# Kernel tuning notes

Hardware: AMD Instinct MI355X
Metric: run time of the kernel (lower is better)

The kernel has to match this reference:

```python
import jax, jax.numpy as jnp
import numpy as np

NUM_OBJECTS = 6          # self.NUM_OBJECTS
SCORE_THRESH = 1e-4      # self.score_tresh
NMS_THRESHS = jnp.asarray(np.arange(0.001, 1.0, 0.1), dtype=jnp.float32)  # 10 thresholds
K_CAND = 1024            # fixed-shape cap on (proposal,class) candidates per image
CLASS_OFFSET = 4096.0    # > max image coord; batched_nms per-class offset trick


def _iou_matrix(b):
    # b: [K,4] xyxy -> [K,K] IoU
    x1, y1, x2, y2 = b[:, 0], b[:, 1], b[:, 2], b[:, 3]
    area = (x2 - x1) * (y2 - y1)
    iw = jnp.clip(jnp.minimum(x2[:, None], x2[None, :]) - jnp.maximum(x1[:, None], x1[None, :]), 0.0)
    ih = jnp.clip(jnp.minimum(y2[:, None], y2[None, :]) - jnp.maximum(y1[:, None], y1[None, :]), 0.0)
    inter = iw * ih
    union = area[:, None] + area[None, :] - inter
    return jnp.where(union > 0, inter / union, 0.0)


def _greedy_nms(iou, valid, thresh):
    # candidates are pre-sorted by descending score; sequential greedy suppression
    K = valid.shape[0]
    ar = jnp.arange(K)
    def body(i, keep):
        sup = keep[i] & (iou[i] > thresh) & (ar > i)
        return keep & ~sup
    return jax.lax.fori_loop(0, K, body, valid)


def _per_image(logits, boxes, feats, hw):
    # logits [N,81], boxes [N,80,4], feats [N,2048], hw [2] (h,w)
    C = boxes.shape[1]
    probs = jax.nn.softmax(logits, axis=-1)[:, :C]          # drop background class
    h = hw[0].astype(boxes.dtype)
    w = hw[1].astype(boxes.dtype)
    b = jnp.stack([jnp.clip(boxes[..., 0], 0.0, w),         # clip to image
                   jnp.clip(boxes[..., 1], 0.0, h),
                   jnp.clip(boxes[..., 2], 0.0, w),
                   jnp.clip(boxes[..., 3], 0.0, h)], axis=-1)
    scores = probs.reshape(-1)                              # [N*C]
    vals, idx = jax.lax.top_k(jnp.where(scores > SCORE_THRESH, scores, -1.0), K_CAND)
    cand_valid = vals > SCORE_THRESH
    cb = b.reshape(-1, 4)[idx]                              # [K,4]
    cls = (idx % C).astype(boxes.dtype)
    prop = idx // C                                         # proposal row index
    iou = _iou_matrix(cb + cls[:, None] * CLASS_OFFSET)     # per-class NMS via offsets
    keeps = jax.vmap(lambda t: _greedy_nms(iou, cand_valid, t))(NMS_THRESHS)  # [T,K]
    counts = keeps.sum(axis=1)
    # torch loop: break at first (smallest) thresh yielding len(ids)==6, i.e. >=6 kept
    ok = counts >= NUM_OBJECTS
    t_sel = jnp.where(jnp.any(ok), jnp.argmax(ok), NMS_THRESHS.shape[0] - 1)
    keep = keeps[t_sel]
    _, top = jax.lax.top_k(jnp.where(keep, vals, -jnp.inf), NUM_OBJECTS)
    ids = prop[top]                                         # [6]
    return feats[ids].T                                     # [2048, 6] (permute(1,0))


def _forward(cls_logits, boxes, feature_pooled, image_hw):
    return jax.vmap(_per_image)(cls_logits, boxes, feature_pooled, image_hw)  # [B,2048,6]


def setup_inputs() -> dict:
    key = jax.random.key(0)
    k1, k2, k3, k4, k5 = jax.random.split(key, 5)
    B, N, C, D = 8, 1000, 80, 2048
    cls_logits = jax.random.normal(k1, (B, N, C + 1), dtype=jnp.float32)
    ctr = jax.random.uniform(k2, (B, N, C, 2), minval=0.0, maxval=800.0)
    sz = jax.random.uniform(k3, (B, N, C, 2), minval=8.0, maxval=200.0)
    boxes = jnp.concatenate([ctr - sz * 0.5, ctr + sz * 0.5], axis=-1).astype(jnp.float32)
    feature_pooled = jax.random.normal(k4, (B, N, D), dtype=jnp.float32)
    image_hw = jax.random.randint(k5, (B, 2), 600, 800, dtype=jnp.int32)
    return {"cls_logits": cls_logits, "boxes": boxes,
            "feature_pooled": feature_pooled, "image_hw": image_hw}


def reference(cls_logits, boxes, feature_pooled, image_hw):
    return _forward(cls_logits, boxes, feature_pooled, image_hw)
```

## Files before the change

kernel.cpp:

```cpp
#include <hip/hip_runtime.h>
#include <cmath>
#include <cstdint>

#define NB 8
#define NPROP 1000
#define NCLS 80
#define NLOG 81
#define KCAND 1024
#define NTH 10
#define DFEAT 2048
#define NOBJ 6
#define NSCORE (NPROP*NCLS)
#define HBLK 8
#define HCHUNK (NSCORE/HBLK)

constexpr size_t OFF_SCORES = 0;
constexpr size_t SZ_SCORES  = (size_t)NB * NSCORE * 4;
constexpr size_t OFF_LISTA  = OFF_SCORES + SZ_SCORES;
constexpr size_t SZ_LISTA   = (size_t)NB * 20 * KCAND * 8;
constexpr size_t OFF_H1     = OFF_LISTA;
constexpr size_t OFF_H2     = OFF_H1 + (size_t)NB * HBLK * 2048 * 4;
constexpr size_t OFF_PIV    = OFF_H2 + (size_t)NB * HBLK * 2048 * 4;
constexpr size_t OFF_CBUF   = OFF_PIV + (size_t)NB * 8 * 4;
constexpr size_t OFF_CANDK  = OFF_LISTA + SZ_LISTA;
constexpr size_t SZ_CANDK   = (size_t)NB * KCAND * 8;
constexpr size_t OFF_CX1    = OFF_CANDK + SZ_CANDK;
constexpr size_t SZ_CARR    = (size_t)NB * KCAND * 4;
constexpr size_t OFF_CY1    = OFF_CX1 + SZ_CARR;
constexpr size_t OFF_CX2    = OFF_CY1 + SZ_CARR;
constexpr size_t OFF_CY2    = OFF_CX2 + SZ_CARR;
constexpr size_t OFF_CAREA  = OFF_CY2 + SZ_CARR;
constexpr size_t OFF_CPROP  = OFF_CAREA + SZ_CARR;
constexpr size_t OFF_VALIDW = OFF_CPROP + SZ_CARR;
constexpr size_t SZ_VALIDW  = (size_t)NB * 16 * 8;
constexpr size_t OFF_MASKS  = OFF_VALIDW + SZ_VALIDW;
constexpr size_t SZ_MASKS   = (size_t)NTH * NB * KCAND * 16 * 8;
constexpr size_t OFF_KEEPS  = OFF_MASKS + SZ_MASKS;
constexpr size_t SZ_KEEPS   = (size_t)NB * NTH * 16 * 8;
constexpr size_t OFF_COUNTS = OFF_KEEPS + SZ_KEEPS;
constexpr size_t SZ_COUNTS  = (size_t)NB * NTH * 4;
constexpr size_t OFF_IDS    = OFF_COUNTS + SZ_COUNTS;

#define TSTRIDE ((size_t)NB * 16 * 1024)

__device__ __forceinline__ float nms_th(int t) {
    return (float)(0.001 + 0.1 * (double)t);
}

__device__ __forceinline__ unsigned score_vkey(float v) {
    float vv = (v > 1e-4f) ? v : -1.0f;
    unsigned bits = __float_as_uint(vv);
    unsigned u = (bits & 0x80000000u) ? ~bits : (bits | 0x80000000u);
    return ~u;
}

__global__ void k_memz(ulonglong2* __restrict__ p, int n) {
    int g = blockIdx.x * blockDim.x + threadIdx.x;
    if (g < n) p[g] = ulonglong2{0ULL, 0ULL};
}

__global__ void k_softmax(const float* __restrict__ logits, float* __restrict__ scores) {
    int wid  = (blockIdx.x * blockDim.x + threadIdx.x) >> 6;
    int lane = threadIdx.x & 63;
    if (wid >= NB * NPROP) return;
    const float* L = logits + (size_t)wid * NLOG;
    float l0 = L[lane];
    float l1 = (lane < 17) ? L[64 + lane] : -INFINITY;
    float m = fmaxf(l0, l1);
    #pragma unroll
    for (int o = 32; o > 0; o >>= 1) m = fmaxf(m, __shfl_xor(m, o, 64));
    float e0 = expf(l0 - m);
    float e1 = (lane < 17) ? expf(l1 - m) : 0.f;
    float s = e0 + e1;
    #pragma unroll
    for (int o = 32; o > 0; o >>= 1) s += __shfl_xor(s, o, 64);
    float* outp = scores + (size_t)wid * NCLS;
    outp[lane] = e0 / s;
    if (lane < 16) outp[64 + lane] = e1 / s;
}

__global__ __launch_bounds__(1024) void k_hist1(const float* __restrict__ scores,
                                                unsigned* __restrict__ hist1) {
    __shared__ unsigned hh[2048];
    int img = blockIdx.x >> 3, blk = blockIdx.x & 7;
    int tid = threadIdx.x;
    hh[tid] = 0; hh[tid + 1024] = 0;
    __syncthreads();
    const float* sc = scores + (size_t)img * NSCORE + (size_t)blk * HCHUNK;
    for (int e = tid; e < HCHUNK; e += 1024) {
        unsigned vk = score_vkey(sc[e]);
        atomicAdd(&hh[vk >> 21], 1u);
    }
    __syncthreads();
    unsigned* outp = hist1 + ((size_t)img * HBLK + blk) * 2048;
    outp[tid] = hh[tid];
    outp[tid + 1024] = hh[tid + 1024];
}

__device__ __forceinline__ void pivot_scan(const unsigned* __restrict__ h8, unsigned K,
                                           int* __restrict__ out_b, int* __restrict__ out_rem) {
    __shared__ unsigned wsum[16];
    int tid = threadIdx.x;
    unsigned a = 0, b = 0;
    #pragma unroll
    for (int s = 0; s < HBLK; ++s) {
        a += h8[s * 2048 + 2 * tid];
        b += h8[s * 2048 + 2 * tid + 1];
    }
    unsigned p = a + b;
    unsigned x = p;
    #pragma unroll
    for (int d = 1; d < 64; d <<= 1) {
        unsigned y = __shfl_up(x, (unsigned)d, 64);
        if ((tid & 63) >= d) x += y;
    }
    if ((tid & 63) == 63) wsum[tid >> 6] = x;
    __syncthreads();
    if (tid < 16) {
        unsigned w = wsum[tid];
        #pragma unroll
        for (int d = 1; d < 16; d <<= 1) {
            unsigned y = __shfl_up(w, (unsigned)d, 64);
            if (tid >= d) w += y;
        }
        wsum[tid] = w;
    }
    __syncthreads();
    unsigned wex = (tid >= 64) ? wsum[(tid >> 6) - 1] : 0u;
    unsigned incl = x + wex;
    unsigned E = incl - p;
    if (E < K && E + a >= K)              { *out_b = 2 * tid;     *out_rem = (int)(K - E); }
    else if (E + a < K && E + a + b >= K) { *out_b = 2 * tid + 1; *out_rem = (int)(K - (E + a)); }
}

__global__ __launch_bounds__(1024) void k_pivot1(const unsigned* __restrict__ hist1,
                                                 int* __restrict__ piv) {
    int img = blockIdx.x;
    pivot_scan(hist1 + (size_t)img * HBLK * 2048, KCAND,
               &piv[img * 8 + 0], &piv[img * 8 + 1]);
}

__global__ __launch_bounds__(1024) void k_hist2(const float* __restrict__ scores,
                                                const int* __restrict__ piv,
                                                unsigned* __restrict__ hist2) {
    __shared__ unsigned hh[2048];
    int img = blockIdx.x >> 3, blk = blockIdx.x & 7;
    int tid = threadIdx.x;
    hh[tid] = 0; hh[tid + 1024] = 0;
    __syncthreads();
    unsigned b1 = (unsigned)piv[img * 8 + 0];
    const float* sc = scores + (size_t)img * NSCORE + (size_t)blk * HCHUNK;
    for (int e = tid; e < HCHUNK; e += 1024) {
        unsigned vk = score_vkey(sc[e]);
        if ((vk >> 21) == b1) atomicAdd(&hh[(vk >> 10) & 2047u], 1u);
    }
    __syncthreads();
    unsigned* outp = hist2 + ((size_t)img * HBLK + blk) * 2048;
    outp[tid] = hh[tid];
    outp[tid + 1024] = hh[tid + 1024];
}

__global__ __launch_bounds__(1024) void k_pivot2(const unsigned* __restrict__ hist2,
                                                 int* __restrict__ piv) {
    __shared__ int b2s, rem2s;
    int img = blockIdx.x;
    pivot_scan(hist2 + (size_t)img * HBLK * 2048, (unsigned)piv[img * 8 + 1], &b2s, &rem2s);
    __syncthreads();
    if (threadIdx.x == 0) {
        piv[img * 8 + 2] = (piv[img * 8 + 0] << 11) | b2s;
        piv[img * 8 + 3] = 0;
    }
}

__global__ __launch_bounds__(1024) void k_gathersel(const float* __restrict__ scores,
                                                    int* __restrict__ piv,
                                                    unsigned long long* __restrict__ cbuf) {
    __shared__ unsigned lcnt, gbase;
    int img = blockIdx.x >> 3, blk = blockIdx.x & 7;
    int tid = threadIdx.x;
    if (tid == 0) lcnt = 0;
    __syncthreads();
    unsigned T22 = (unsigned)piv[img * 8 + 2];
    const float* sc = scores + (size_t)img * NSCORE + (size_t)blk * HCHUNK;
    unsigned long long sel[(HCHUNK + 1023) / 1024];
    int ns = 0;
    for (int e = tid; e < HCHUNK; e += 1024) {
        unsigned vk = score_vkey(sc[e]);
        if ((vk >> 10) <= T22)
            sel[ns++] = ((unsigned long long)vk << 32) | (unsigned)(blk * HCHUNK + e);
    }
    unsigned lp = atomicAdd(&lcnt, (unsigned)ns);
    __syncthreads();
    if (tid == 0) gbase = atomicAdd((unsigned*)&piv[img * 8 + 3], lcnt);
    __syncthreads();
    unsigned long long* ob = cbuf + (size_t)img * 2048;
    for (int i = 0; i < ns; ++i) {
        unsigned pos = gbase + lp + (unsigned)i;
        if (pos < 2048) ob[pos] = sel[i];
    }
}

__global__ __launch_bounds__(256) void k_rank(const unsigned long long* __restrict__ cbuf,
                                              const int* __restrict__ piv,
                                              unsigned long long* __restrict__ candk) {
    __shared__ unsigned long long keys[2048];
    int img = blockIdx.x >> 3, sl = blockIdx.x & 7;
    int tid = threadIdx.x;
    int cnt = piv[img * 8 + 3]; if (cnt > 2048) cnt = 2048;
    const unsigned long long* ib = cbuf + (size_t)img * 2048;
    #pragma unroll
    for (int k = 0; k < 8; ++k) {
        int t = k * 256 + tid;
        keys[t] = (t < cnt) ? ib[t] : ~0ULL;
    }
    __syncthreads();
    unsigned long long a = keys[sl * 256 + tid];
    int r = 0;
    #pragma unroll 8
    for (int j = 0; j < cnt; ++j) r += (keys[j] < a) ? 1 : 0;
    if (r < KCAND) candk[(size_t)img * KCAND + r] = a;
}

__global__ __launch_bounds__(1024) void k_cand(const unsigned long long* __restrict__ candk,
                                               const float* __restrict__ boxes,
                                               const int* __restrict__ hw,
                                               float* __restrict__ cx1, float* __restrict__ cy1,
                                               float* __restrict__ cx2, float* __restrict__ cy2,
                                               float* __restrict__ car, int* __restrict__ cprop,
                                               unsigned long long* __restrict__ validw) {
    int bimg = blockIdx.x;
    int j    = threadIdx.x;
    unsigned long long key = candk[(size_t)bimg * KCAND + j];
    unsigned int u   = ~(unsigned int)(key >> 32);
    unsigned int idx = (unsigned int)key;
    const unsigned int uth = __float_as_uint(1e-4f) | 0x80000000u;
    bool valid = u > uth;
    int prop = (int)(idx / NCLS);
    int cls  = (int)(idx - (unsigned)prop * NCLS);
    const float4 bx = *(const float4*)(boxes + ((((size_t)bimg * NPROP + prop) * NCLS + cls) << 2));
    float h = (float)hw[bimg * 2 + 0];
    float w = (float)hw[bimg * 2 + 1];
    float x1 = fminf(fmaxf(bx.x, 0.f), w);
    float y1 = fminf(fmaxf(bx.y, 0.f), h);
    float x2 = fminf(fmaxf(bx.z, 0.f), w);
    float y2 = fminf(fmaxf(bx.w, 0.f), h);
    float offc = __fmul_rn((float)cls, 4096.0f);
    x1 = __fadd_rn(x1, offc); y1 = __fadd_rn(y1, offc);
    x2 = __fadd_rn(x2, offc); y2 = __fadd_rn(y2, offc);
    float area = __fmul_rn(__fsub_rn(x2, x1), __fsub_rn(y2, y1));
    int o = bimg * KCAND + j;
    cx1[o] = x1; cy1[o] = y1; cx2[o] = x2; cy2[o] = y2; car[o] = area; cprop[o] = prop;
    unsigned long long bal = __ballot(valid);
    if ((threadIdx.x & 63) == 0) validw[bimg * 16 + (j >> 6)] = bal;
}

__global__ void k_masks(const float* __restrict__ cx1, const float* __restrict__ cy1,
                        const float* __restrict__ cx2, const float* __restrict__ cy2,
                        const float* __restrict__ car,
                        unsigned long long* __restrict__ masks) {
    int gw   = (blockIdx.x * blockDim.x + threadIdx.x) >> 6;
    int lane = threadIdx.x & 63;
    if (gw >= NB * KCAND) return;
    int bimg = gw >> 10;
    int i    = gw & (KCAND - 1);
    int cb   = bimg * KCAND;
    float xi1 = cx1[cb + i], yi1 = cy1[cb + i];
    float xi2 = cx2[cb + i], yi2 = cy2[cb + i], ai = car[cb + i];
    int cmax = i >> 6;
    for (int c = 0; c <= cmax; ++c) {
        int j = c * 64 + lane;
        float xj1 = cx1[cb + j], yj1 = cy1[cb + j];
        float xj2 = cx2[cb + j], yj2 = cy2[cb + j], aj = car[cb + j];
        float iw = fmaxf(__fsub_rn(fminf(xi2, xj2), fmaxf(xi1, xj1)), 0.f);
        float ih = fmaxf(__fsub_rn(fminf(yi2, yj2), fmaxf(yi1, yj1)), 0.f);
        float inter = __fmul_rn(iw, ih);
        bool jlt = j < i;
        if (__ballot(jlt && (inter > 0.f)) == 0ULL) continue;
        float uni = __fsub_rn(__fadd_rn(ai, aj), inter);
        float iou = (uni > 0.f) ? __fdiv_rn(inter, uni) : 0.f;
        unsigned long long bl[NTH];
        #pragma unroll
        for (int t = 0; t < NTH; ++t) bl[t] = __ballot(jlt && (iou > nms_th(t)));
        unsigned long long myv = 0;
        #pragma unroll
        for (int t = 0; t < NTH; ++t) myv = (lane == t) ? bl[t] : myv;
        if (lane < NTH)
            masks[(size_t)lane * TSTRIDE + (((size_t)(bimg * 16 + c)) << 10) + i] = myv;
    }
}

__global__ __launch_bounds__(1024) void k_scan(const unsigned long long* __restrict__ masks,
                                               const unsigned long long* __restrict__ validw,
                                               unsigned long long* __restrict__ keeps,
                                               int* __restrict__ counts) {
    __shared__ unsigned long long kp[16];
    __shared__ int changed[2];
    int bt   = blockIdx.x;
    int bimg = bt / NTH, t = bt % NTH;
    int tid  = threadIdx.x;
    int w    = tid >> 6;
    int lane = tid & 63;
    const unsigned long long* mb = masks + (size_t)t * TSTRIDE + ((size_t)(bimg * 16) << 10);
    unsigned long long row[16];
    #pragma unroll
    for (int c = 0; c < 16; ++c)
        row[c] = (c <= w) ? mb[((size_t)c << 10) + tid] : 0ULL;
    unsigned long long vw = validw[bimg * 16 + w];
    bool valid = (vw >> lane) & 1ULL;
    if (tid < 16) kp[tid] = validw[bimg * 16 + tid];
    if (tid < 2) changed[tid] = 0;
    __syncthreads();
    for (int iter = 0; iter < KCAND + 2; ++iter) {
        unsigned long long s = 0;
        #pragma unroll
        for (int c = 0; c < 16; ++c) s |= row[c] & kp[c];
        bool nk = valid && (s == 0);
        unsigned long long bal = __ballot(nk);
        bool diff = (lane == 0) && (bal != kp[w]);
        __syncthreads();
        if (diff) { kp[w] = bal; changed[iter & 1] = 1; }
        if (tid == 0) changed[(iter + 1) & 1] = 0;
        __syncthreads();
        if (!changed[iter & 1]) break;
    }
    if (tid < 16) keeps[((size_t)bimg * NTH + t) * 16 + tid] = kp[tid];
    if (tid < 64) {
        int c = (lane < 16) ? __popcll(kp[lane]) : 0;
        #pragma unroll
        for (int o = 32; o > 0; o >>= 1) c += __shfl_xor(c, o, 64);
        if (lane == 0) counts[bimg * NTH + t] = c;
    }
}

__global__ void k_select(const int* __restrict__ counts,
                         const unsigned long long* __restrict__ keeps,
                         const int* __restrict__ cprop, int* __restrict__ ids) {
    int bimg = blockIdx.x;
    if (threadIdx.x != 0) return;
    int tsel = NTH - 1;
    for (int t = 0; t < NTH; ++t) {
        if (counts[bimg * NTH + t] >= NOBJ) { tsel = t; break; }
    }
    const unsigned long long* kw = keeps + ((size_t)bimg * NTH + tsel) * 16;
    int got = 0;
    for (int k = 0; k < 16 && got < NOBJ; ++k) {
        unsigned long long x = kw[k];
        while (x && got < NOBJ) {
            int b = __builtin_ctzll(x);
            ids[bimg * NOBJ + got] = cprop[bimg * KCAND + k * 64 + b];
            ++got;
            x &= x - 1;
        }
    }
    for (int k = 0; k < 16 && got < NOBJ; ++k) {
        unsigned long long x = ~kw[k];
        while (x && got < NOBJ) {
            int b = __builtin_ctzll(x);
            ids[bimg * NOBJ + got] = cprop[bimg * KCAND + k * 64 + b];
            ++got;
            x &= x - 1;
        }
    }
}

__global__ void k_featgather(const float* __restrict__ feats, const int* __restrict__ ids,
                             float* __restrict__ outp) {
    int g = blockIdx.x * blockDim.x + threadIdx.x;
    if (g >= NB * DFEAT) return;
    int bimg = g / DFEAT;
    int d    = g - bimg * DFEAT;
    const float* fb = feats + (size_t)bimg * NPROP * DFEAT;
    float* ob = outp + ((size_t)bimg * DFEAT + d) * NOBJ;
    #pragma unroll
    for (int s = 0; s < NOBJ; ++s) {
        int id = ids[bimg * NOBJ + s];
        ob[s] = fb[(size_t)id * DFEAT + d];
    }
}

extern "C" void kernel_launch(void* const* d_in, const int* in_sizes, int n_in,
                              void* d_out, int out_size, void* d_ws, size_t ws_size,
                              hipStream_t stream) {
    const float* logits = (const float*)d_in[0];
    const float* boxes  = (const float*)d_in[1];
    const float* feats  = (const float*)d_in[2];
    const int*   hw     = (const int*)d_in[3];
    float* outp = (float*)d_out;

    char* ws = (char*)d_ws;
    float*              scores = (float*)(ws + OFF_SCORES);
    unsigned*           hist1  = (unsigned*)(ws + OFF_H1);
    unsigned*           hist2  = (unsigned*)(ws + OFF_H2);
    int*                piv    = (int*)(ws + OFF_PIV);
    unsigned long long* cbuf   = (unsigned long long*)(ws + OFF_CBUF);
    unsigned long long* candk  = (unsigned long long*)(ws + OFF_CANDK);
    float* cx1 = (float*)(ws + OFF_CX1);
    float* cy1 = (float*)(ws + OFF_CY1);
    float* cx2 = (float*)(ws + OFF_CX2);
    float* cy2 = (float*)(ws + OFF_CY2);
    float* car = (float*)(ws + OFF_CAREA);
    int*   cprop = (int*)(ws + OFF_CPROP);
    unsigned long long* validw = (unsigned long long*)(ws + OFF_VALIDW);
    unsigned long long* masks  = (unsigned long long*)(ws + OFF_MASKS);
    unsigned long long* keeps  = (unsigned long long*)(ws + OFF_KEEPS);
    int* counts = (int*)(ws + OFF_COUNTS);
    int* ids    = (int*)(ws + OFF_IDS);

    const int mz_n = (int)(SZ_MASKS / 16);
    k_memz<<<(mz_n + 255) / 256, 256, 0, stream>>>((ulonglong2*)masks, mz_n);
    k_softmax<<<(NB * NPROP) / 4, 256, 0, stream>>>(logits, scores);
    k_hist1<<<NB * HBLK, 1024, 0, stream>>>(scores, hist1);
    k_pivot1<<<NB, 1024, 0, stream>>>(hist1, piv);
    k_hist2<<<NB * HBLK, 1024, 0, stream>>>(scores, piv, hist2);
    k_pivot2<<<NB, 1024, 0, stream>>>(hist2, piv);
    k_gathersel<<<NB * HBLK, 1024, 0, stream>>>(scores, piv, cbuf);
    k_rank<<<NB * HBLK, 256, 0, stream>>>(cbuf, piv, candk);
    k_cand<<<NB, 1024, 0, stream>>>(candk, boxes, hw, cx1, cy1, cx2, cy2, car, cprop, validw);
    k_masks<<<(NB * KCAND) / 4, 256, 0, stream>>>(cx1, cy1, cx2, cy2, car, masks);
    k_scan<<<NB * NTH, 1024, 0, stream>>>(masks, validw, keeps, counts);
    k_select<<<NB, 64, 0, stream>>>(counts, keeps, cprop, ids);
    k_featgather<<<(NB * DFEAT + 255) / 256, 256, 0, stream>>>(feats, ids, outp);
}
```

Before: 168.6 us.

## Fuse top-k selection pipeline kernels and skip cross-class IoU chunks

Folds the pipeline from 13 launches into 8. Softmax now runs together with the first histogram, each pivot scan runs inside the kernel that consumes it, ranking is combined with candidate box preparation, and selection is combined with the feature gather. The mask kernel also stores each candidate's class and skips 64-wide chunks where no earlier candidate shares the row's class, avoiding IoU work on pairs that the class offset already separates. In exchange, every histogram block repeats the pivot scan, the valid-bit words are built with global atomicOr and need zeroing first, and every select block repeats the serial id selection.

After: 169.4 us. About the same (+0.5%).

```diff
diff --git a/kernel.cpp b/kernel.cpp
--- a/kernel.cpp
+++ b/kernel.cpp
@@ -13,6 +13,7 @@
 #define NSCORE (NPROP*NCLS)
 #define HBLK 8
 #define HCHUNK (NSCORE/HBLK)
+#define PCHUNK (NPROP/HBLK)
 
 constexpr size_t OFF_SCORES = 0;
 constexpr size_t SZ_SCORES  = (size_t)NB * NSCORE * 4;
@@ -39,7 +40,8 @@
 constexpr size_t SZ_KEEPS   = (size_t)NB * NTH * 16 * 8;
 constexpr size_t OFF_COUNTS = OFF_KEEPS + SZ_KEEPS;
 constexpr size_t SZ_COUNTS  = (size_t)NB * NTH * 4;
-constexpr size_t OFF_IDS    = OFF_COUNTS + SZ_COUNTS;
+constexpr size_t OFF_CCLS   = OFF_COUNTS + SZ_COUNTS;
+constexpr size_t SZ_CCLS    = (size_t)NB * KCAND * 4;
 
 #define TSTRIDE ((size_t)NB * 16 * 1024)
 
@@ -59,37 +61,36 @@
     if (g < n) p[g] = ulonglong2{0ULL, 0ULL};
 }
 
-__global__ void k_softmax(const float* __restrict__ logits, float* __restrict__ scores) {
-    int wid  = (blockIdx.x * blockDim.x + threadIdx.x) >> 6;
-    int lane = threadIdx.x & 63;
-    if (wid >= NB * NPROP) return;
-    const float* L = logits + (size_t)wid * NLOG;
-    float l0 = L[lane];
-    float l1 = (lane < 17) ? L[64 + lane] : -INFINITY;
-    float m = fmaxf(l0, l1);
-    #pragma unroll
-    for (int o = 32; o > 0; o >>= 1) m = fmaxf(m, __shfl_xor(m, o, 64));
-    float e0 = expf(l0 - m);
-    float e1 = (lane < 17) ? expf(l1 - m) : 0.f;
-    float s = e0 + e1;
-    #pragma unroll
-    for (int o = 32; o > 0; o >>= 1) s += __shfl_xor(s, o, 64);
-    float* outp = scores + (size_t)wid * NCLS;
-    outp[lane] = e0 / s;
-    if (lane < 16) outp[64 + lane] = e1 / s;
-}
-
-__global__ __launch_bounds__(1024) void k_hist1(const float* __restrict__ scores,
-                                                unsigned* __restrict__ hist1) {
+__global__ __launch_bounds__(1024) void k_softhist(const float* __restrict__ logits,
+                                                   float* __restrict__ scores,
+                                                   unsigned* __restrict__ hist1) {
     __shared__ unsigned hh[2048];
     int img = blockIdx.x >> 3, blk = blockIdx.x & 7;
-    int tid = threadIdx.x;
+    int tid = threadIdx.x, wid = tid >> 6, lane = tid & 63;
     hh[tid] = 0; hh[tid + 1024] = 0;
     __syncthreads();
-    const float* sc = scores + (size_t)img * NSCORE + (size_t)blk * HCHUNK;
-    for (int e = tid; e < HCHUNK; e += 1024) {
-        unsigned vk = score_vkey(sc[e]);
-        atomicAdd(&hh[vk >> 21], 1u);
+    for (int p = wid; p < PCHUNK; p += 16) {
+        int prop = blk * PCHUNK + p;
+        const float* L = logits + ((size_t)img * NPROP + prop) * NLOG;
+        float l0 = L[lane];
+        float l1 = (lane < 17) ? L[64 + lane] : -INFINITY;
+        float m = fmaxf(l0, l1);
+        #pragma unroll
+        for (int o = 32; o > 0; o >>= 1) m = fmaxf(m, __shfl_xor(m, o, 64));
+        float e0 = expf(l0 - m);
+        float e1 = (lane < 17) ? expf(l1 - m) : 0.f;
+        float s = e0 + e1;
+        #pragma unroll
+        for (int o = 32; o > 0; o >>= 1) s += __shfl_xor(s, o, 64);
+        float* op = scores + ((size_t)img * NPROP + prop) * NCLS;
+        float p0 = e0 / s;
+        op[lane] = p0;
+        atomicAdd(&hh[score_vkey(p0) >> 21], 1u);
+        if (lane < 16) {
+            float p1 = e1 / s;
+            op[64 + lane] = p1;
+            atomicAdd(&hh[score_vkey(p1) >> 21], 1u);
+        }
     }
     __syncthreads();
     unsigned* outp = hist1 + ((size_t)img * HBLK + blk) * 2048;
@@ -133,22 +134,18 @@
     else if (E + a < K && E + a + b >= K) { *out_b = 2 * tid + 1; *out_rem = (int)(K - (E + a)); }
 }
 
-__global__ __launch_bounds__(1024) void k_pivot1(const unsigned* __restrict__ hist1,
+__global__ __launch_bounds__(1024) void k_hist2p(const float* __restrict__ scores,
+                                                 const unsigned* __restrict__ hist1,
+                                                 unsigned* __restrict__ hist2,
                                                  int* __restrict__ piv) {
-    int img = blockIdx.x;
-    pivot_scan(hist1 + (size_t)img * HBLK * 2048, KCAND,
-               &piv[img * 8 + 0], &piv[img * 8 + 1]);
-}
-
-__global__ __launch_bounds__(1024) void k_hist2(const float* __restrict__ scores,
-                                                const int* __restrict__ piv,
-                                                unsigned* __restrict__ hist2) {
     __shared__ unsigned hh[2048];
+    __shared__ int sb, sr;
     int img = blockIdx.x >> 3, blk = blockIdx.x & 7;
     int tid = threadIdx.x;
     hh[tid] = 0; hh[tid + 1024] = 0;
-    __syncthreads();
-    unsigned b1 = (unsigned)piv[img * 8 + 0];
+    pivot_scan(hist1 + (size_t)img * HBLK * 2048, KCAND, &sb, &sr);
+    __syncthreads();
+    unsigned b1 = (unsigned)sb;
     const float* sc = scores + (size_t)img * NSCORE + (size_t)blk * HCHUNK;
     for (int e = tid; e < HCHUNK; e += 1024) {
         unsigned vk = score_vkey(sc[e]);
@@ -158,29 +155,26 @@
     unsigned* outp = hist2 + ((size_t)img * HBLK + blk) * 2048;
     outp[tid] = hh[tid];
     outp[tid + 1024] = hh[tid + 1024];
-}
-
-__global__ __launch_bounds__(1024) void k_pivot2(const unsigned* __restrict__ hist2,
-                                                 int* __restrict__ piv) {
-    __shared__ int b2s, rem2s;
-    int img = blockIdx.x;
-    pivot_scan(hist2 + (size_t)img * HBLK * 2048, (unsigned)piv[img * 8 + 1], &b2s, &rem2s);
-    __syncthreads();
-    if (threadIdx.x == 0) {
-        piv[img * 8 + 2] = (piv[img * 8 + 0] << 11) | b2s;
+    if (blk == 0 && tid == 0) {
+        piv[img * 8 + 0] = sb;
+        piv[img * 8 + 1] = sr;
         piv[img * 8 + 3] = 0;
     }
 }
 
-__global__ __launch_bounds__(1024) void k_gathersel(const float* __restrict__ scores,
-                                                    int* __restrict__ piv,
-                                                    unsigned long long* __restrict__ cbuf) {
+__global__ __launch_bounds__(1024) void k_gatherp(const float* __restrict__ scores,
+                                                  const unsigned* __restrict__ hist2,
+                                                  int* __restrict__ piv,
+                                                  unsigned long long* __restrict__ cbuf) {
+    __shared__ int sb2, sr2;
     __shared__ unsigned lcnt, gbase;
     int img = blockIdx.x >> 3, blk = blockIdx.x & 7;
     int tid = threadIdx.x;
     if (tid == 0) lcnt = 0;
-    __syncthreads();
-    unsigned T22 = (unsigned)piv[img * 8 + 2];
+    unsigned K2 = (unsigned)piv[img * 8 + 1];
+    pivot_scan(hist2 + (size_t)img * HBLK * 2048, K2, &sb2, &sr2);
+    __syncthreads();
+    unsigned T22 = ((unsigned)piv[img * 8 + 0] << 11) | (unsigned)sb2;
     const float* sc = scores + (size_t)img * NSCORE + (size_t)blk * HCHUNK;
     unsigned long long sel[(HCHUNK + 1023) / 1024];
     int ns = 0;
@@ -200,9 +194,15 @@
     }
 }
 
-__global__ __launch_bounds__(256) void k_rank(const unsigned long long* __restrict__ cbuf,
-                                              const int* __restrict__ piv,
-                                              unsigned long long* __restrict__ candk) {
+__global__ __launch_bounds__(256) void k_rankcand(const unsigned long long* __restrict__ cbuf,
+                                                  const int* __restrict__ piv,
+                                                  const float* __restrict__ boxes,
+                                                  const int* __restrict__ hw,
+                                                  float* __restrict__ cx1, float* __restrict__ cy1,
+                                                  float* __restrict__ cx2, float* __restrict__ cy2,
+                                                  float* __restrict__ car, int* __restrict__ cprop,
+                                                  int* __restrict__ ccls,
+                                                  unsigned long long* __restrict__ validw) {
     __shared__ unsigned long long keys[2048];
     int img = blockIdx.x >> 3, sl = blockIdx.x & 7;
     int tid = threadIdx.x;
@@ -218,45 +218,34 @@
     int r = 0;
     #pragma unroll 8
     for (int j = 0; j < cnt; ++j) r += (keys[j] < a) ? 1 : 0;
-    if (r < KCAND) candk[(size_t)img * KCAND + r] = a;
-}
-
-__global__ __launch_bounds__(1024) void k_cand(const unsigned long long* __restrict__ candk,
-                                               const float* __restrict__ boxes,
-                                               const int* __restrict__ hw,
-                                               float* __restrict__ cx1, float* __restrict__ cy1,
-                                               float* __restrict__ cx2, float* __restrict__ cy2,
-                                               float* __restrict__ car, int* __restrict__ cprop,
-                                               unsigned long long* __restrict__ validw) {
-    int bimg = blockIdx.x;
-    int j    = threadIdx.x;
-    unsigned long long key = candk[(size_t)bimg * KCAND + j];
-    unsigned int u   = ~(unsigned int)(key >> 32);
-    unsigned int idx = (unsigned int)key;
-    const unsigned int uth = __float_as_uint(1e-4f) | 0x80000000u;
-    bool valid = u > uth;
-    int prop = (int)(idx / NCLS);
-    int cls  = (int)(idx - (unsigned)prop * NCLS);
-    const float4 bx = *(const float4*)(boxes + ((((size_t)bimg * NPROP + prop) * NCLS + cls) << 2));
-    float h = (float)hw[bimg * 2 + 0];
-    float w = (float)hw[bimg * 2 + 1];
-    float x1 = fminf(fmaxf(bx.x, 0.f), w);
-    float y1 = fminf(fmaxf(bx.y, 0.f), h);
-    float x2 = fminf(fmaxf(bx.z, 0.f), w);
-    float y2 = fminf(fmaxf(bx.w, 0.f), h);
-    float offc = __fmul_rn((float)cls, 4096.0f);
-    x1 = __fadd_rn(x1, offc); y1 = __fadd_rn(y1, offc);
-    x2 = __fadd_rn(x2, offc); y2 = __fadd_rn(y2, offc);
-    float area = __fmul_rn(__fsub_rn(x2, x1), __fsub_rn(y2, y1));
-    int o = bimg * KCAND + j;
-    cx1[o] = x1; cy1[o] = y1; cx2[o] = x2; cy2[o] = y2; car[o] = area; cprop[o] = prop;
-    unsigned long long bal = __ballot(valid);
-    if ((threadIdx.x & 63) == 0) validw[bimg * 16 + (j >> 6)] = bal;
+    if (r < KCAND) {
+        unsigned u   = ~(unsigned)(a >> 32);
+        unsigned idx = (unsigned)a;
+        const unsigned uth = __float_as_uint(1e-4f) | 0x80000000u;
+        bool valid = u > uth;
+        int prop = (int)(idx / NCLS);
+        int cls  = (int)(idx - (unsigned)prop * NCLS);
+        const float4 bx = *(const float4*)(boxes + ((((size_t)img * NPROP + prop) * NCLS + cls) << 2));
+        float h = (float)hw[img * 2 + 0];
+        float w = (float)hw[img * 2 + 1];
+        float x1 = fminf(fmaxf(bx.x, 0.f), w);
+        float y1 = fminf(fmaxf(bx.y, 0.f), h);
+        float x2 = fminf(fmaxf(bx.z, 0.f), w);
+        float y2 = fminf(fmaxf(bx.w, 0.f), h);
+        float offc = __fmul_rn((float)cls, 4096.0f);
+        x1 = __fadd_rn(x1, offc); y1 = __fadd_rn(y1, offc);
+        x2 = __fadd_rn(x2, offc); y2 = __fadd_rn(y2, offc);
+        float area = __fmul_rn(__fsub_rn(x2, x1), __fsub_rn(y2, y1));
+        int o = img * KCAND + r;
+        cx1[o] = x1; cy1[o] = y1; cx2[o] = x2; cy2[o] = y2;
+        car[o] = area; cprop[o] = prop; ccls[o] = cls;
+        if (valid) atomicOr(&validw[img * 16 + (r >> 6)], 1ULL << (r & 63));
+    }
 }
 
 __global__ void k_masks(const float* __restrict__ cx1, const float* __restrict__ cy1,
                         const float* __restrict__ cx2, const float* __restrict__ cy2,
-                        const float* __restrict__ car,
+                        const float* __restrict__ car, const int* __restrict__ ccls,
                         unsigned long long* __restrict__ masks) {
     int gw   = (blockIdx.x * blockDim.x + threadIdx.x) >> 6;
     int lane = threadIdx.x & 63;
@@ -264,17 +253,20 @@
     int bimg = gw >> 10;
     int i    = gw & (KCAND - 1);
     int cb   = bimg * KCAND;
+    int   ci  = ccls[cb + i];
     float xi1 = cx1[cb + i], yi1 = cy1[cb + i];
     float xi2 = cx2[cb + i], yi2 = cy2[cb + i], ai = car[cb + i];
     int cmax = i >> 6;
     for (int c = 0; c <= cmax; ++c) {
         int j = c * 64 + lane;
+        bool jlt = j < i;
+        int cj = ccls[cb + j];
+        if (__ballot(jlt && (cj == ci)) == 0ULL) continue;
         float xj1 = cx1[cb + j], yj1 = cy1[cb + j];
         float xj2 = cx2[cb + j], yj2 = cy2[cb + j], aj = car[cb + j];
         float iw = fmaxf(__fsub_rn(fminf(xi2, xj2), fmaxf(xi1, xj1)), 0.f);
         float ih = fmaxf(__fsub_rn(fminf(yi2, yj2), fmaxf(yi1, yj1)), 0.f);
         float inter = __fmul_rn(iw, ih);
-        bool jlt = j < i;
         if (__ballot(jlt && (inter > 0.f)) == 0ULL) continue;
         float uni = __fsub_rn(__fadd_rn(ai, aj), inter);
         float iou = (uni > 0.f) ? __fdiv_rn(inter, uni) : 0.f;
@@ -332,50 +324,53 @@
     }
 }
 
-__global__ void k_select(const int* __restrict__ counts,
-                         const unsigned long long* __restrict__ keeps,
-                         const int* __restrict__ cprop, int* __restrict__ ids) {
-    int bimg = blockIdx.x;
-    if (threadIdx.x != 0) return;
-    int tsel = NTH - 1;
-    for (int t = 0; t < NTH; ++t) {
-        if (counts[bimg * NTH + t] >= NOBJ) { tsel = t; break; }
-    }
-    const unsigned long long* kw = keeps + ((size_t)bimg * NTH + tsel) * 16;
-    int got = 0;
-    for (int k = 0; k < 16 && got < NOBJ; ++k) {
-        unsigned long long x = kw[k];
-        while (x && got < NOBJ) {
-            int b = __builtin_ctzll(x);
-            ids[bimg * NOBJ + got] = cprop[bimg * KCAND + k * 64 + b];
-            ++got;
-            x &= x - 1;
+__global__ __launch_bounds__(256) void k_selfeat(const int* __restrict__ counts,
+                                                 const unsigned long long* __restrict__ keeps,
+                                                 const int* __restrict__ cprop,
+                                                 const float* __restrict__ feats,
+                                                 float* __restrict__ outp) {
+    __shared__ int scnt[NTH];
+    __shared__ unsigned long long skw[16];
+    __shared__ int stsel;
+    __shared__ int sids[NOBJ];
+    int img = blockIdx.x >> 3;
+    int tid = threadIdx.x;
+    if (tid < NTH) scnt[tid] = counts[img * NTH + tid];
+    __syncthreads();
+    if (tid == 0) {
+        int tsel = NTH - 1;
+        for (int t = 0; t < NTH; ++t) if (scnt[t] >= NOBJ) { tsel = t; break; }
+        stsel = tsel;
+    }
+    __syncthreads();
+    if (tid < 16) skw[tid] = keeps[((size_t)img * NTH + stsel) * 16 + tid];
+    __syncthreads();
+    if (tid == 0) {
+        int got = 0;
+        for (int k = 0; k < 16 && got < NOBJ; ++k) {
+            unsigned long long x = skw[k];
+            while (x && got < NOBJ) {
+                int b = __builtin_ctzll(x);
+                sids[got++] = cprop[img * KCAND + k * 64 + b];
+                x &= x - 1;
+            }
         }
-    }
-    for (int k = 0; k < 16 && got < NOBJ; ++k) {
-        unsigned long long x = ~kw[k];
-        while (x && got < NOBJ) {
-            int b = __builtin_ctzll(x);
-            ids[bimg * NOBJ + got] = cprop[bimg * KCAND + k * 64 + b];
-            ++got;
-            x &= x - 1;
+        for (int k = 0; k < 16 && got < NOBJ; ++k) {
+            unsigned long long x = ~skw[k];
+            while (x && got < NOBJ) {
+                int b = __builtin_ctzll(x);
+                sids[got++] = cprop[img * KCAND + k * 64 + b];
+                x &= x - 1;
+            }
         }
     }
-}
-
-__global__ void k_featgather(const float* __restrict__ feats, const int* __restrict__ ids,
-                             float* __restrict__ outp) {
-    int g = blockIdx.x * blockDim.x + threadIdx.x;
-    if (g >= NB * DFEAT) return;
-    int bimg = g / DFEAT;
-    int d    = g - bimg * DFEAT;
-    const float* fb = feats + (size_t)bimg * NPROP * DFEAT;
-    float* ob = outp + ((size_t)bimg * DFEAT + d) * NOBJ;
+    __syncthreads();
+    int d = (blockIdx.x & 7) * 256 + tid;
+    const float* fb = feats + (size_t)img * NPROP * DFEAT;
+    float* ob = outp + ((size_t)img * DFEAT + d) * NOBJ;
     #pragma unroll
-    for (int s = 0; s < NOBJ; ++s) {
-        int id = ids[bimg * NOBJ + s];
-        ob[s] = fb[(size_t)id * DFEAT + d];
-    }
+    for (int s = 0; s < NOBJ; ++s)
+        ob[s] = fb[(size_t)sids[s] * DFEAT + d];
 }
 
 extern "C" void kernel_launch(void* const* d_in, const int* in_sizes, int n_in,
@@ -393,31 +388,26 @@
     unsigned*           hist2  = (unsigned*)(ws + OFF_H2);
     int*                piv    = (int*)(ws + OFF_PIV);
     unsigned long long* cbuf   = (unsigned long long*)(ws + OFF_CBUF);
-    unsigned long long* candk  = (unsigned long long*)(ws + OFF_CANDK);
     float* cx1 = (float*)(ws + OFF_CX1);
     float* cy1 = (float*)(ws + OFF_CY1);
     float* cx2 = (float*)(ws + OFF_CX2);
     float* cy2 = (float*)(ws + OFF_CY2);
     float* car = (float*)(ws + OFF_CAREA);
     int*   cprop = (int*)(ws + OFF_CPROP);
+    int*   ccls  = (int*)(ws + OFF_CCLS);
     unsigned long long* validw = (unsigned long long*)(ws + OFF_VALIDW);
     unsigned long long* masks  = (unsigned long long*)(ws + OFF_MASKS);
     unsigned long long* keeps  = (unsigned long long*)(ws + OFF_KEEPS);
     int* counts = (int*)(ws + OFF_COUNTS);
-    int* ids    = (int*)(ws + OFF_IDS);
-
-    const int mz_n = (int)(SZ_MASKS / 16);
-    k_memz<<<(mz_n + 255) / 256, 256, 0, stream>>>((ulonglong2*)masks, mz_n);
-    k_softmax<<<(NB * NPROP) / 4, 256, 0, stream>>>(logits, scores);
-    k_hist1<<<NB * HBLK, 1024, 0, stream>>>(scores, hist1);
-    k_pivot1<<<NB, 1024, 0, stream>>>(hist1, piv);
-    k_hist2<<<NB * HBLK, 1024, 0, stream>>>(scores, piv, hist2);
-    k_pivot2<<<NB, 1024, 0, stream>>>(hist2, piv);
-    k_gathersel<<<NB * HBLK, 1024, 0, stream>>>(scores, piv, cbuf);
-    k_rank<<<NB * HBLK, 256, 0, stream>>>(cbuf, piv, candk);
-    k_cand<<<NB, 1024, 0, stream>>>(candk, boxes, hw, cx1, cy1, cx2, cy2, car, cprop, validw);
-    k_masks<<<(NB * KCAND) / 4, 256, 0, stream>>>(cx1, cy1, cx2, cy2, car, masks);
+
+    const int mz_n = (int)((SZ_VALIDW + SZ_MASKS) / 16);
+    k_memz<<<(mz_n + 255) / 256, 256, 0, stream>>>((ulonglong2*)(ws + OFF_VALIDW), mz_n);
+    k_softhist<<<NB * HBLK, 1024, 0, stream>>>(logits, scores, hist1);
+    k_hist2p<<<NB * HBLK, 1024, 0, stream>>>(scores, hist1, hist2, piv);
+    k_gatherp<<<NB * HBLK, 1024, 0, stream>>>(scores, hist2, piv, cbuf);
+    k_rankcand<<<NB * HBLK, 256, 0, stream>>>(cbuf, piv, boxes, hw,
+                                              cx1, cy1, cx2, cy2, car, cprop, ccls, validw);
+    k_masks<<<(NB * KCAND) / 4, 256, 0, stream>>>(cx1, cy1, cx2, cy2, car, ccls, masks);
     k_scan<<<NB * NTH, 1024, 0, stream>>>(masks, validw, keeps, counts);
-    k_select<<<NB, 64, 0, stream>>>(counts, keeps, cprop, ids);
-    k_featgather<<<(NB * DFEAT + 255) / 256, 256, 0, stream>>>(feats, ids, outp);
-}
+    k_selfeat<<<NB * HBLK, 256, 0, stream>>>(counts, keeps, cprop, feats, outp);
+}
```
